# Kernel optimization log

Hardware: AMD Instinct MI355X
Metric: run time of the kernel (lower is better)

The kernel has to match this reference:

```python
import jax, jax.numpy as jnp
import numpy as np

DIM = 2048; H = 16; QLR = 512; KVLR = 512
NOPE = 128; ROPE = 64; VHD = 128
QKHD = NOPE + ROPE
SCALE = QKHD ** -0.5
EPS = 1.1920929e-07  # torch RMSNorm default eps = finfo(float32).eps
B = 1; S = 2048

def _rmsnorm(x, w):
    return x * jax.lax.rsqrt(jnp.mean(x * x, axis=-1, keepdims=True) + EPS) * w

def _rope(x, cos, sin):
    # x: [b, s, h, d]; cos/sin: [s, d//2] (consecutive-pair complex rotation)
    b, s, h, d = x.shape
    x2 = x.reshape(b, s, h, d // 2, 2)
    x0, x1 = x2[..., 0], x2[..., 1]
    c = cos[None, :, None, :]; sn = sin[None, :, None, :]
    y = jnp.stack([x0 * c - x1 * sn, x0 * sn + x1 * c], axis=-1)
    return y.reshape(b, s, h, d)

def setup_inputs() -> dict:
    key = jax.random.key(0)
    ks = jax.random.split(key, 12)
    def lin(k, fan_in, fan_out):
        bound = 1.0 / np.sqrt(fan_in)
        kw, kb = jax.random.split(k)
        w = jax.random.uniform(kw, (fan_out, fan_in), jnp.float32, -bound, bound)
        b = jax.random.uniform(kb, (fan_out,), jnp.float32, -bound, bound)
        return w, b
    x = jax.random.normal(ks[0], (B, S, DIM), jnp.float32)
    theta = jax.random.uniform(ks[1], (S, ROPE // 2), jnp.float32, 0.0, 2 * np.pi)
    freqs_cos = jnp.cos(theta); freqs_sin = jnp.sin(theta)
    mask = jnp.where(jnp.triu(jnp.ones((S, S), bool), k=1), jnp.float32(-1e9), jnp.float32(0.0))
    wq_a_w, wq_a_b = lin(ks[2], DIM, QLR)
    q_norm_w = jnp.ones((QLR,), jnp.float32)
    wq_b_w, wq_b_b = lin(ks[3], QLR, H * QKHD)
    wkv_a_w, wkv_a_b = lin(ks[4], DIM, KVLR + ROPE)
    kv_norm_w = jnp.ones((KVLR,), jnp.float32)
    wkv_b_w, wkv_b_b = lin(ks[5], KVLR, H * (NOPE + VHD))
    wo_w, wo_b = lin(ks[6], H * VHD, DIM)
    return {"x": x, "start_pos": 0, "freqs_cos": freqs_cos, "freqs_sin": freqs_sin,
            "mask": mask, "wq_a_w": wq_a_w, "wq_a_b": wq_a_b, "q_norm_w": q_norm_w,
            "wq_b_w": wq_b_w, "wq_b_b": wq_b_b, "wkv_a_w": wkv_a_w, "wkv_a_b": wkv_a_b,
            "kv_norm_w": kv_norm_w, "wkv_b_w": wkv_b_w, "wkv_b_b": wkv_b_b,
            "wo_w": wo_w, "wo_b": wo_b}

def reference(x, start_pos, freqs_cos, freqs_sin, mask,
              wq_a_w, wq_a_b, q_norm_w, wq_b_w, wq_b_b,
              wkv_a_w, wkv_a_b, kv_norm_w, wkv_b_w, wkv_b_b, wo_w, wo_b):
    bsz, seqlen, _ = x.shape
    # low-rank query: wq_b(q_norm(wq_a(x)))
    q = _rmsnorm(x @ wq_a_w.T + wq_a_b, q_norm_w) @ wq_b_w.T + wq_b_b
    q = q.reshape(bsz, seqlen, H, QKHD)
    q_nope, q_pe = q[..., :NOPE], q[..., NOPE:]
    q_pe = _rope(q_pe, freqs_cos, freqs_sin)
    kv = x @ wkv_a_w.T + wkv_a_b
    kv_lat, k_pe = kv[..., :KVLR], kv[..., KVLR:]
    k_pe = _rope(k_pe[:, :, None, :], freqs_cos, freqs_sin)  # [b,s,1,ROPE]
    q = jnp.concatenate([q_nope, q_pe], axis=-1)
    kvb = (_rmsnorm(kv_lat, kv_norm_w) @ wkv_b_w.T + wkv_b_b).reshape(bsz, seqlen, H, NOPE + VHD)
    k_nope, v = kvb[..., :NOPE], kvb[..., NOPE:]
    k = jnp.concatenate([k_nope, jnp.broadcast_to(k_pe, (bsz, seqlen, H, ROPE))], axis=-1)
    # prefill (start_pos=0): cache[:end_pos] == freshly written k/v
    scores = jnp.einsum('bshd,bthd->bsht', q, k) * SCALE
    scores = scores + mask[None, :, None, :]
    probs = jax.nn.softmax(scores.astype(jnp.float32), axis=-1).astype(x.dtype)
    out = jnp.einsum('bsht,bthd->bshd', probs, v).reshape(bsz, seqlen, H * VHD)
    return out @ wo_w.T + wo_b
```

## Files before the change

### kernel.cpp

```cpp
#include <hip/hip_runtime.h>
#include <hip/hip_bf16.h>

typedef __attribute__((ext_vector_type(8))) short short8x;
typedef __attribute__((ext_vector_type(4))) short short4x;
typedef __attribute__((ext_vector_type(4))) float float4x;
typedef __hip_bfloat16 bf16;

#define EPS_F 1.1920929e-07f
#define SCALE_F 0.07216878364870323f

__device__ inline float rdv(const void* p, size_t i, int f32) {
  return f32 ? ((const float*)p)[i] : __bfloat162float(((const bf16*)p)[i]);
}

__device__ inline int4 pack8(const float* s) {
  unsigned short h[8];
#pragma unroll
  for (int t = 0; t < 8; t++) {
    bf16 b = __float2bfloat16(s[t]);
    __builtin_memcpy(&h[t], &b, 2);
  }
  int4 r;
  r.x = (int)((unsigned)h[0] | ((unsigned)h[1] << 16));
  r.y = (int)((unsigned)h[2] | ((unsigned)h[3] << 16));
  r.z = (int)((unsigned)h[4] | ((unsigned)h[5] << 16));
  r.w = (int)((unsigned)h[6] | ((unsigned)h[7] << 16));
  return r;
}

typedef __attribute__((address_space(1))) const unsigned int gu32;
typedef __attribute__((address_space(3))) unsigned int lu32;
__device__ __forceinline__ void gload16(const void* g, void* l) {
  __builtin_amdgcn_global_load_lds((gu32*)g, (lu32*)l, 16, 0, 0);
}

__global__ __launch_bounds__(256) void detect_dtype(const unsigned short* __restrict__ x,
                                                    int* __restrict__ flag) {
  int tid = threadIdx.x;
  int cnt = 0;
#pragma unroll
  for (int i = 0; i < 4; i++) {
    unsigned short u = x[tid * 4 + i];
    int e = (u >> 7) & 0xFF;
    cnt += (e >= 118 && e <= 130) ? 1 : 0;
  }
#pragma unroll
  for (int off = 1; off < 64; off <<= 1) cnt += __shfl_xor(cnt, off);
  __shared__ int red[4];
  if ((tid & 63) == 0) red[tid >> 6] = cnt;
  __syncthreads();
  if (tid == 0) flag[0] = ((red[0] + red[1] + red[2] + red[3]) > 768) ? 0 : 1;
}

__global__ __launch_bounds__(256) void sentinel_kernel(bf16* out, int n) {
  int i = blockIdx.x * 256 + threadIdx.x;
  if (i < n) out[i] = __float2bfloat16(1000.0f);
}

template<int OMODE, bool A_DYN>
__device__ __forceinline__ void gemm128_body(
    const void* __restrict__ A, const void* __restrict__ W,
    const void* __restrict__ bias, void* __restrict__ Cout,
    int M, int N, int K, int f32in, int bx, int by,
    int kbeg, int kend, int addbias)
{
  __shared__ int4 As4[128 * 4];
  __shared__ int4 Bs4[128 * 4];
  const int tid = threadIdx.x, lane = tid & 63, wave = tid >> 6;
  const int grp = lane >> 4, l16 = lane & 15;
  const int m0 = bx * 128, n0 = by * 128;
  const int wm = (wave & 1) * 64, wn = (wave >> 1) * 64;
  float4x acc[4][4] = {};
  for (int k0 = kbeg; k0 < kend; k0 += 32) {
    if (!f32in) {
#pragma unroll
      for (int j = 0; j < 2; j++) {
        int row = wave * 32 + j * 16 + (lane >> 2);
        int cs = (lane & 3) ^ ((row >> 1) & 3);
        gload16((const bf16*)A + (size_t)(m0 + row) * K + k0 + cs * 8,
                &As4[(wave * 32 + j * 16) * 4]);
        gload16((const bf16*)W + (size_t)(n0 + row) * K + k0 + cs * 8,
                &Bs4[(wave * 32 + j * 16) * 4]);
      }
    } else {
#pragma unroll
      for (int i = 0; i < 2; i++) {
        int ch = tid + i * 256;
        int row = ch >> 2, c = ch & 3;
        int cs = c ^ ((row >> 1) & 3);
        size_t aoff = (size_t)(m0 + row) * K + k0 + cs * 8;
        size_t boff = (size_t)(n0 + row) * K + k0 + cs * 8;
        As4[row * 4 + c] = A_DYN ? pack8((const float*)A + aoff)
                                 : *(const int4*)((const bf16*)A + aoff);
        Bs4[row * 4 + c] = pack8((const float*)W + boff);
      }
    }
    __syncthreads();
    short8x af[4], bfr[4];
#pragma unroll
    for (int i = 0; i < 4; i++) {
      int ra = wm + i * 16 + l16;
      int rb = wn + i * 16 + l16;
      af[i]  = *(const short8x*)&As4[ra * 4 + (grp ^ ((ra >> 1) & 3))];
      bfr[i] = *(const short8x*)&Bs4[rb * 4 + (grp ^ ((rb >> 1) & 3))];
    }
#pragma unroll
    for (int i = 0; i < 4; i++)
#pragma unroll
      for (int j = 0; j < 4; j++)
        acc[i][j] = __builtin_amdgcn_mfma_f32_16x16x32_bf16(af[i], bfr[j], acc[i][j], 0, 0, 0);
    __syncthreads();
  }
#pragma unroll
  for (int j = 0; j < 4; j++) {
    int gn = n0 + wn + j * 16 + l16;
    float bv = addbias ? rdv(bias, gn, f32in) : 0.0f;
#pragma unroll
    for (int i = 0; i < 4; i++) {
      int gm0 = m0 + wm + i * 16 + grp * 4;
#pragma unroll
      for (int r = 0; r < 4; r++) {
        float v = acc[i][j][r] + bv;
        size_t idx = (size_t)(gm0 + r) * N + gn;
        if (OMODE == 0)      ((float*)Cout)[idx] = v;
        else if (OMODE == 1) ((bf16*)Cout)[idx] = __float2bfloat16(v);
        else {
          if (f32in) ((float*)Cout)[idx] = v;
          else       ((bf16*)Cout)[idx] = __float2bfloat16(v);
        }
      }
    }
  }
}

__global__ __launch_bounds__(256) void gemmB_dual(
    const void* __restrict__ A0, const void* __restrict__ A1,
    const void* __restrict__ W0, const void* __restrict__ W1,
    const void* __restrict__ b0, const void* __restrict__ b1,
    void* __restrict__ C0, void* __restrict__ C1,
    const int* __restrict__ flagp)
{
  const int z = blockIdx.z;
  if (z == 0 && blockIdx.y >= 24) return;
  const void* A = z ? A1 : A0;
  const void* W = z ? W1 : W0;
  const void* bias = z ? b1 : b0;
  void* C = z ? C1 : C0;
  const int N = z ? 4096 : 3072;
  gemm128_body<1, false>(A, W, bias, C, 2048, N, 512, flagp[0],
                         blockIdx.x, blockIdx.y, 0, 512, 1);
}

__global__ __launch_bounds__(256) void gemmWo_sk(
    const void* __restrict__ A, const void* __restrict__ W,
    const void* __restrict__ bias, float* __restrict__ part,
    const int* __restrict__ flagp)
{
  const int z = blockIdx.z;
  gemm128_body<0, false>(A, W, bias, part + (size_t)z * 2048 * 2048,
                         2048, 2048, 2048, flagp[0],
                         blockIdx.x, blockIdx.y, z * 1024, z * 1024 + 1024, z == 0);
}

__global__ __launch_bounds__(256) void reduce_out(
    const float* __restrict__ p0, const float* __restrict__ p1,
    void* __restrict__ out, const int* __restrict__ flagp)
{
  const int f32in = flagp[0];
  size_t i = ((size_t)blockIdx.x * 256 + threadIdx.x) * 4;
  float4 a = *(const float4*)(p0 + i);
  float4 b = *(const float4*)(p1 + i);
  a.x += b.x; a.y += b.y; a.z += b.z; a.w += b.w;
  if (f32in) {
    *(float4*)((float*)out + i) = a;
  } else {
    unsigned short h[4];
    bf16 t0 = __float2bfloat16(a.x); __builtin_memcpy(&h[0], &t0, 2);
    bf16 t1 = __float2bfloat16(a.y); __builtin_memcpy(&h[1], &t1, 2);
    bf16 t2 = __float2bfloat16(a.z); __builtin_memcpy(&h[2], &t2, 2);
    bf16 t3 = __float2bfloat16(a.w); __builtin_memcpy(&h[3], &t3, 2);
    int2 v;
    v.x = (int)((unsigned)h[0] | ((unsigned)h[1] << 16));
    v.y = (int)((unsigned)h[2] | ((unsigned)h[3] << 16));
    *(int2*)((bf16*)out + i) = v;
  }
}

template<int OMODE, bool A_DYN>
__device__ __forceinline__ void gemm64_body(
    const void* __restrict__ A, const void* __restrict__ W,
    const void* __restrict__ bias, void* __restrict__ Cout,
    int M, int N, int K, int f32in, int bx, int by,
    int kbeg, int kend, int addbias)
{
  __shared__ int4 As4[64 * 4];
  __shared__ int4 Bs4[64 * 4];
  const int tid = threadIdx.x, lane = tid & 63, wave = tid >> 6;
  const int grp = lane >> 4, l16 = lane & 15;
  const int m0 = bx * 64, n0 = by * 64;
  const int wm = (wave & 1) * 32, wn = (wave >> 1) * 32;
  float4x acc[2][2] = {};
  for (int k0 = kbeg; k0 < kend; k0 += 32) {
    if (!f32in) {
      int row = wave * 16 + (lane >> 2);
      int cs = (lane & 3) ^ ((row >> 1) & 3);
      gload16((const bf16*)A + (size_t)(m0 + row) * K + k0 + cs * 8,
              &As4[wave * 16 * 4]);
      gload16((const bf16*)W + (size_t)(n0 + row) * K + k0 + cs * 8,
              &Bs4[wave * 16 * 4]);
    } else {
      int row = tid >> 2, c = tid & 3;
      int cs = c ^ ((row >> 1) & 3);
      size_t aoff = (size_t)(m0 + row) * K + k0 + cs * 8;
      size_t boff = (size_t)(n0 + row) * K + k0 + cs * 8;
      As4[row * 4 + c] = A_DYN ? pack8((const float*)A + aoff)
                               : *(const int4*)((const bf16*)A + aoff);
      Bs4[row * 4 + c] = pack8((const float*)W + boff);
    }
    __syncthreads();
    short8x af[2], bfr[2];
#pragma unroll
    for (int i = 0; i < 2; i++) {
      int ra = wm + i * 16 + l16;
      int rb = wn + i * 16 + l16;
      af[i]  = *(const short8x*)&As4[ra * 4 + (grp ^ ((ra >> 1) & 3))];
      bfr[i] = *(const short8x*)&Bs4[rb * 4 + (grp ^ ((rb >> 1) & 3))];
    }
#pragma unroll
    for (int i = 0; i < 2; i++)
#pragma unroll
      for (int j = 0; j < 2; j++)
        acc[i][j] = __builtin_amdgcn_mfma_f32_16x16x32_bf16(af[i], bfr[j], acc[i][j], 0, 0, 0);
    __syncthreads();
  }
#pragma unroll
  for (int j = 0; j < 2; j++) {
    int gn = n0 + wn + j * 16 + l16;
    float bv = addbias ? rdv(bias, gn, f32in) : 0.0f;
#pragma unroll
    for (int i = 0; i < 2; i++) {
      int gm0 = m0 + wm + i * 16 + grp * 4;
#pragma unroll
      for (int r = 0; r < 4; r++) {
        float v = acc[i][j][r] + bv;
        size_t idx = (size_t)(gm0 + r) * N + gn;
        if (OMODE == 0)      ((float*)Cout)[idx] = v;
        else if (OMODE == 1) ((bf16*)Cout)[idx] = __float2bfloat16(v);
        else {
          if (f32in) ((float*)Cout)[idx] = v;
          else       ((bf16*)Cout)[idx] = __float2bfloat16(v);
        }
      }
    }
  }
}

__global__ __launch_bounds__(256) void gemmA_sk(
    const void* __restrict__ A,
    const void* __restrict__ W0, const void* __restrict__ W1,
    const void* __restrict__ b0, const void* __restrict__ b1,
    float* __restrict__ C0, float* __restrict__ C1,
    const int* __restrict__ flagp)
{
  const int z = blockIdx.z;
  const int mat = z >> 1, kh = z & 1;
  const int N = mat ? 576 : 512;
  if (blockIdx.y * 64 >= N) return;
  const void* W = mat ? W1 : W0;
  const void* bias = mat ? b1 : b0;
  float* C = (mat ? C1 : C0) + (size_t)kh * 2048 * N;
  gemm64_body<0, true>(A, W, bias, C, 2048, N, 2048, flagp[0],
                       blockIdx.x, blockIdx.y,
                       kh * 1024, kh * 1024 + 1024, kh == 0);
}

__global__ __launch_bounds__(256) void norms_merged(
    const float* __restrict__ q_a0, const float* __restrict__ q_a1,
    const float* __restrict__ kv_a0, const float* __restrict__ kv_a1,
    const void* __restrict__ qw, const void* __restrict__ kvw,
    const void* __restrict__ cosb, const void* __restrict__ sinb,
    bf16* __restrict__ qn, bf16* __restrict__ kvn, bf16* __restrict__ kpe,
    const int* __restrict__ flagp)
{
  const int f32in = flagp[0];
  const int b = blockIdx.x, tid = threadIdx.x;
  __shared__ float red[4];
  if (b < 2048) {
    const int s = b;
    size_t base = (size_t)s * 512;
    float v0 = q_a0[base + tid] + q_a1[base + tid];
    float v1 = q_a0[base + tid + 256] + q_a1[base + tid + 256];
    float ss = v0 * v0 + v1 * v1;
#pragma unroll
    for (int off = 1; off < 64; off <<= 1) ss += __shfl_xor(ss, off);
    if ((tid & 63) == 0) red[tid >> 6] = ss;
    __syncthreads();
    float tot = red[0] + red[1] + red[2] + red[3];
    float scale = rsqrtf(tot * (1.0f / 512.0f) + EPS_F);
    qn[base + tid]       = __float2bfloat16(v0 * scale * rdv(qw, tid, f32in));
    qn[base + tid + 256] = __float2bfloat16(v1 * scale * rdv(qw, tid + 256, f32in));
  } else {
    const int s = b - 2048;
    size_t base = (size_t)s * 576;
    float v0 = kv_a0[base + tid] + kv_a1[base + tid];
    float v1 = kv_a0[base + tid + 256] + kv_a1[base + tid + 256];
    float ss = v0 * v0 + v1 * v1;
#pragma unroll
    for (int off = 1; off < 64; off <<= 1) ss += __shfl_xor(ss, off);
    if ((tid & 63) == 0) red[tid >> 6] = ss;
    __syncthreads();
    float tot = red[0] + red[1] + red[2] + red[3];
    float scale = rsqrtf(tot * (1.0f / 512.0f) + EPS_F);
    kvn[(size_t)s * 512 + tid]       = __float2bfloat16(v0 * scale * rdv(kvw, tid, f32in));
    kvn[(size_t)s * 512 + tid + 256] = __float2bfloat16(v1 * scale * rdv(kvw, tid + 256, f32in));
    if (tid < 32) {
      float x0 = kv_a0[base + 512 + 2 * tid] + kv_a1[base + 512 + 2 * tid];
      float x1 = kv_a0[base + 512 + 2 * tid + 1] + kv_a1[base + 512 + 2 * tid + 1];
      float c  = rdv(cosb, (size_t)s * 32 + tid, f32in);
      float sn = rdv(sinb, (size_t)s * 32 + tid, f32in);
      kpe[s * 64 + 2 * tid]     = __float2bfloat16(x0 * c - x1 * sn);
      kpe[s * 64 + 2 * tid + 1] = __float2bfloat16(x0 * sn + x1 * c);
    }
  }
}

__global__ __launch_bounds__(256) void rope_vt_merged(
    bf16* __restrict__ q, const void* __restrict__ cosb,
    const void* __restrict__ sinb, const bf16* __restrict__ kvb,
    bf16* __restrict__ Vt, const int* __restrict__ flagp)
{
  const int b = blockIdx.x, tid = threadIdx.x;
  __shared__ __align__(16) bf16 tile[64][136];
  if (b < 2048) {
    const int f32in = flagp[0];
    const int s = b;
#pragma unroll
    for (int it = 0; it < 2; it++) {
      int p = tid + it * 256;
      int hh = p >> 5, jj = p & 31;
      bf16* src = q + (size_t)s * 3072 + hh * 192 + 128 + 2 * jj;
      float x0 = __bfloat162float(src[0]);
      float x1 = __bfloat162float(src[1]);
      float c  = rdv(cosb, (size_t)s * 32 + jj, f32in);
      float sn = rdv(sinb, (size_t)s * 32 + jj, f32in);
      src[0] = __float2bfloat16(x0 * c - x1 * sn);
      src[1] = __float2bfloat16(x0 * sn + x1 * c);
    }
  } else {
    const int hb = b - 2048;
    const int h = hb & 15;
    const int t0 = (hb >> 4) * 64;
#pragma unroll
    for (int i = 0; i < 4; i++) {
      int chunk = tid + i * 256;
      int row = chunk >> 4;
      int c8 = (chunk & 15) * 8;
      *(int4*)&tile[row][c8] =
          *(const int4*)(kvb + (size_t)(t0 + row) * 4096 + h * 256 + 128 + c8);
    }
    __syncthreads();
#pragma unroll
    for (int i = 0; i < 32; i++) {
      int idx = tid + i * 256;
      int d = idx >> 6;
      int t = idx & 63;
      Vt[((size_t)h * 128 + d) * 2048 + t0 + t] = tile[t][d];
    }
  }
}

__global__ __launch_bounds__(256) void attn_kernel(
    const bf16* __restrict__ Q, const bf16* __restrict__ kvb,
    const bf16* __restrict__ kpe, const bf16* __restrict__ Vt,
    bf16* __restrict__ Out)
{
  __shared__ __align__(16) bf16 Ks[64 * 200];
  __shared__ __align__(16) bf16 Vs[128 * 72];
  __shared__ __align__(16) bf16 plds[4][16 * 68];
  const int b = blockIdx.x;
  const int h = b & 15;
  const int tt = (b >> 4) & 15;
  const int q0 = ((b >> 8) ? (31 - tt) : tt) * 64;
  const int tid = threadIdx.x;
  const int wave = tid >> 6;
  const int lane = tid & 63;
  const int grp = lane >> 4, l16 = lane & 15;
  const int qrt = q0 + wave * 16;
  const bf16* Qbase = Q + (size_t)(qrt + l16) * 3072 + h * 192;
  short8x qf[6];
#pragma unroll
  for (int c = 0; c < 6; c++)
    qf[c] = *(const short8x*)(Qbase + c * 32 + grp * 8);
  float m_run[4], l_run[4];
  float4x o_acc[8] = {};
#pragma unroll
  for (int r = 0; r < 4; r++) { m_run[r] = -__builtin_inff(); l_run[r] = 0.f; }
  bf16* pl = &plds[wave][0];
  for (int t0 = 0; t0 <= q0; t0 += 64) {
#pragma unroll
    for (int i = 0; i < 4; i++) {
      int ch = tid + i * 256;
      int row = ch >> 4, c = ch & 15;
      *(int4*)&Ks[row * 200 + c * 8] =
          *(const int4*)(kvb + (size_t)(t0 + row) * 4096 + h * 256 + c * 8);
    }
#pragma unroll
    for (int i = 0; i < 2; i++) {
      int ch = tid + i * 256;
      int row = ch >> 3, c = ch & 7;
      *(int4*)&Ks[row * 200 + 128 + c * 8] =
          *(const int4*)(kpe + (size_t)(t0 + row) * 64 + c * 8);
    }
#pragma unroll
    for (int i = 0; i < 4; i++) {
      int ch = tid + i * 256;
      int row = ch >> 3, c = ch & 7;
      *(int4*)&Vs[row * 72 + c * 8] =
          *(const int4*)(Vt + ((size_t)h * 128 + row) * 2048 + t0 + c * 8);
    }
    __syncthreads();
    float4x sacc[4] = {};
#pragma unroll
    for (int n = 0; n < 4; n++) {
      const bf16* Kb = &Ks[(n * 16 + l16) * 200 + grp * 8];
#pragma unroll
      for (int c = 0; c < 6; c++) {
        short8x kf = *(const short8x*)(Kb + c * 32);
        sacc[n] = __builtin_amdgcn_mfma_f32_16x16x32_bf16(qf[c], kf, sacc[n], 0, 0, 0);
      }
    }
    float pv[4][4], alpha[4];
#pragma unroll
    for (int r = 0; r < 4; r++) {
      const int s_row = qrt + grp * 4 + r;
      float p0[4];
      float mx = -__builtin_inff();
#pragma unroll
      for (int n = 0; n < 4; n++) {
        int t = t0 + n * 16 + l16;
        float v = sacc[n][r] * SCALE_F;
        v = (t > s_row) ? -1.0e9f : v;
        p0[n] = v;
        mx = fmaxf(mx, v);
      }
      mx = fmaxf(mx, __shfl_xor(mx, 1));
      mx = fmaxf(mx, __shfl_xor(mx, 2));
      mx = fmaxf(mx, __shfl_xor(mx, 4));
      mx = fmaxf(mx, __shfl_xor(mx, 8));
      float m_new = fmaxf(m_run[r], mx);
      float a = __expf(m_run[r] - m_new);
      m_run[r] = m_new;
      float sum = 0.f;
#pragma unroll
      for (int n = 0; n < 4; n++) {
        float e = __expf(p0[n] - m_new);
        pv[n][r] = e;
        sum += e;
      }
      sum += __shfl_xor(sum, 1);
      sum += __shfl_xor(sum, 2);
      sum += __shfl_xor(sum, 4);
      sum += __shfl_xor(sum, 8);
      l_run[r] = l_run[r] * a + sum;
      alpha[r] = a;
    }
#pragma unroll
    for (int n = 0; n < 8; n++)
#pragma unroll
      for (int r = 0; r < 4; r++)
        o_acc[n][r] *= alpha[r];
#pragma unroll
    for (int n = 0; n < 4; n++)
#pragma unroll
      for (int r = 0; r < 4; r++)
        pl[(grp * 4 + r) * 68 + n * 16 + l16] = __float2bfloat16(pv[n][r]);
#pragma unroll
    for (int c = 0; c < 2; c++) {
      union { short4x h4[2]; short8x v8; } pk;
      const bf16* pp = pl + l16 * 68 + c * 32 + grp * 8;
      pk.h4[0] = *(const short4x*)(pp);
      pk.h4[1] = *(const short4x*)(pp + 4);
#pragma unroll
      for (int n = 0; n < 8; n++) {
        short8x vf = *(const short8x*)&Vs[(size_t)(n * 16 + l16) * 72 + c * 32 + grp * 8];
        o_acc[n] = __builtin_amdgcn_mfma_f32_16x16x32_bf16(pk.v8, vf, o_acc[n], 0, 0, 0);
      }
    }
    __syncthreads();
  }
  float inv[4];
#pragma unroll
  for (int r = 0; r < 4; r++) inv[r] = 1.0f / l_run[r];
#pragma unroll
  for (int n = 0; n < 8; n++)
#pragma unroll
    for (int r = 0; r < 4; r++) {
      int s_row = qrt + grp * 4 + r;
      Out[(size_t)s_row * 2048 + h * 128 + n * 16 + l16] =
          __float2bfloat16(o_acc[n][r] * inv[r]);
    }
}

extern "C" void kernel_launch(void* const* d_in, const int* in_sizes, int n_in,
                              void* d_out, int out_size, void* d_ws, size_t ws_size,
                              hipStream_t stream) {
  const void* x        = d_in[0];
  const void* fcos     = d_in[2];
  const void* fsin     = d_in[3];
  const void* wq_a_w   = d_in[5];
  const void* wq_a_b   = d_in[6];
  const void* q_norm_w = d_in[7];
  const void* wq_b_w   = d_in[8];
  const void* wq_b_b   = d_in[9];
  const void* wkv_a_w  = d_in[10];
  const void* wkv_a_b  = d_in[11];
  const void* kv_norm_w= d_in[12];
  const void* wkv_b_w  = d_in[13];
  const void* wkv_b_b  = d_in[14];
  const void* wo_w     = d_in[15];
  const void* wo_b     = d_in[16];

  const size_t KB = 1024, MB = 1024 * 1024;
  if (ws_size < 46 * MB) {
    sentinel_kernel<<<(out_size + 255) / 256, 256, 0, stream>>>((bf16*)d_out, out_size);
    return;
  }
  char* ws = (char*)d_ws;
  bf16*  kpe    = (bf16*)(ws);
  int*   flag   = (int*)(ws + 256 * KB);
  bf16*  qbuf   = (bf16*)(ws + 512 * KB);
  bf16*  kvb    = (bf16*)(ws + 12 * MB + 512 * KB);
  bf16*  Vt     = (bf16*)(ws + 28 * MB + 512 * KB);
  bf16*  attnout= (bf16*)(ws + 36 * MB + 512 * KB);
  float* kv_a0  = (float*)(ws + 512 * KB);
  float* kv_a1  = (float*)(ws + 5 * MB);
  float* q_a0   = (float*)(ws + 36 * MB + 512 * KB);
  float* q_a1   = (float*)(ws + 40 * MB + 512 * KB);
  bf16*  qn     = (bf16*)(ws + 28 * MB + 512 * KB);
  bf16*  kvn    = (bf16*)(ws + 30 * MB + 512 * KB);
  float* wpart  = (float*)(ws + 512 * KB);

  dim3 blk(256);
  detect_dtype<<<1, blk, 0, stream>>>((const unsigned short*)x, flag);
  gemmA_sk<<<dim3(32, 9, 4), blk, 0, stream>>>(
      x, wq_a_w, wkv_a_w, wq_a_b, wkv_a_b, q_a0, kv_a0, flag);
  norms_merged<<<4096, blk, 0, stream>>>(
      q_a0, q_a1, kv_a0, kv_a1, q_norm_w, kv_norm_w, fcos, fsin,
      qn, kvn, kpe, flag);
  gemmB_dual<<<dim3(16, 32, 2), blk, 0, stream>>>(
      qn, kvn, wq_b_w, wkv_b_w, wq_b_b, wkv_b_b, qbuf, kvb, flag);
  rope_vt_merged<<<2560, blk, 0, stream>>>(qbuf, fcos, fsin, kvb, Vt, flag);
  attn_kernel<<<dim3(512), blk, 0, stream>>>(qbuf, kvb, kpe, Vt, attnout);
  gemmWo_sk<<<dim3(16, 16, 2), blk, 0, stream>>>(attnout, wo_w, wo_b, wpart, flag);
  reduce_out<<<4096, blk, 0, stream>>>(wpart, wpart + (size_t)2048 * 2048, d_out, flag);
}
```

Measured before the change: 349.2 us.

## Prefetch next K/V tile into registers and use lazy softmax rescaling in attention

The attention loop now issues global loads for the next K, k_pe and V tile into registers before computing on the current tile, then writes them to shared memory after the PV MFMAs. This hides global load latency behind compute. The online softmax rescales the output accumulator only when some row max grows by more than 8, which skips most alpha multiplies at the cost of bounded fp32 growth. The change also adds s_setprio around the MFMA sections and launch_bounds(256,2), which raise register pressure and add an extra barrier per iteration.

```diff
diff --git a/kernel.cpp b/kernel.cpp
--- a/kernel.cpp
+++ b/kernel.cpp
@@ -369,7 +369,7 @@
   }
 }
 
-__global__ __launch_bounds__(256) void attn_kernel(
+__global__ __launch_bounds__(256, 2) void attn_kernel(
     const bf16* __restrict__ Q, const bf16* __restrict__ kvb,
     const bf16* __restrict__ kpe, const bf16* __restrict__ Vt,
     bf16* __restrict__ Out)
@@ -386,40 +386,56 @@
   const int lane = tid & 63;
   const int grp = lane >> 4, l16 = lane & 15;
   const int qrt = q0 + wave * 16;
+  const int krow = tid >> 4, kcol8 = (tid & 15) * 8;
+  const int prow = tid >> 3, pcol8 = (tid & 7) * 8;
+
   const bf16* Qbase = Q + (size_t)(qrt + l16) * 3072 + h * 192;
   short8x qf[6];
 #pragma unroll
   for (int c = 0; c < 6; c++)
     qf[c] = *(const short8x*)(Qbase + c * 32 + grp * 8);
+
+  int4 kReg[4], peReg[2], vReg[4];
+
+  auto attn_issue = [&](int T0) {
+#pragma unroll
+    for (int i = 0; i < 4; i++)
+      kReg[i] = *(const int4*)(kvb + (size_t)(T0 + krow + i * 16) * 4096 + h * 256 + kcol8);
+#pragma unroll
+    for (int i = 0; i < 2; i++)
+      peReg[i] = *(const int4*)(kpe + (size_t)(T0 + prow + i * 32) * 64 + pcol8);
+#pragma unroll
+    for (int i = 0; i < 4; i++)
+      vReg[i] = *(const int4*)(Vt + ((size_t)h * 128 + prow + i * 32) * 2048 + T0 + pcol8);
+  };
+  auto attn_write = [&]() {
+#pragma unroll
+    for (int i = 0; i < 4; i++)
+      *(int4*)&Ks[(krow + i * 16) * 200 + kcol8] = kReg[i];
+#pragma unroll
+    for (int i = 0; i < 2; i++)
+      *(int4*)&Ks[(prow + i * 32) * 200 + 128 + pcol8] = peReg[i];
+#pragma unroll
+    for (int i = 0; i < 4; i++)
+      *(int4*)&Vs[(prow + i * 32) * 72 + pcol8] = vReg[i];
+  };
+
   float m_run[4], l_run[4];
   float4x o_acc[8] = {};
 #pragma unroll
   for (int r = 0; r < 4; r++) { m_run[r] = -__builtin_inff(); l_run[r] = 0.f; }
   bf16* pl = &plds[wave][0];
+
+  attn_issue(0);
+  attn_write();
+  __syncthreads();
+
   for (int t0 = 0; t0 <= q0; t0 += 64) {
-#pragma unroll
-    for (int i = 0; i < 4; i++) {
-      int ch = tid + i * 256;
-      int row = ch >> 4, c = ch & 15;
-      *(int4*)&Ks[row * 200 + c * 8] =
-          *(const int4*)(kvb + (size_t)(t0 + row) * 4096 + h * 256 + c * 8);
-    }
-#pragma unroll
-    for (int i = 0; i < 2; i++) {
-      int ch = tid + i * 256;
-      int row = ch >> 3, c = ch & 7;
-      *(int4*)&Ks[row * 200 + 128 + c * 8] =
-          *(const int4*)(kpe + (size_t)(t0 + row) * 64 + c * 8);
-    }
-#pragma unroll
-    for (int i = 0; i < 4; i++) {
-      int ch = tid + i * 256;
-      int row = ch >> 3, c = ch & 7;
-      *(int4*)&Vs[row * 72 + c * 8] =
-          *(const int4*)(Vt + ((size_t)h * 128 + row) * 2048 + t0 + c * 8);
-    }
-    __syncthreads();
+    const bool more = (t0 + 64 <= q0);
+    if (more) attn_issue(t0 + 64);
+
     float4x sacc[4] = {};
+    __builtin_amdgcn_s_setprio(1);
 #pragma unroll
     for (int n = 0; n < 4; n++) {
       const bf16* Kb = &Ks[(n * 16 + l16) * 200 + grp * 8];
@@ -429,31 +445,51 @@
         sacc[n] = __builtin_amdgcn_mfma_f32_16x16x32_bf16(qf[c], kf, sacc[n], 0, 0, 0);
       }
     }
-    float pv[4][4], alpha[4];
+    __builtin_amdgcn_s_setprio(0);
+
+    float p0[4][4], mxv[4];
+    int grow = 0;
 #pragma unroll
     for (int r = 0; r < 4; r++) {
       const int s_row = qrt + grp * 4 + r;
-      float p0[4];
       float mx = -__builtin_inff();
 #pragma unroll
       for (int n = 0; n < 4; n++) {
         int t = t0 + n * 16 + l16;
         float v = sacc[n][r] * SCALE_F;
         v = (t > s_row) ? -1.0e9f : v;
-        p0[n] = v;
+        p0[r][n] = v;
         mx = fmaxf(mx, v);
       }
       mx = fmaxf(mx, __shfl_xor(mx, 1));
       mx = fmaxf(mx, __shfl_xor(mx, 2));
       mx = fmaxf(mx, __shfl_xor(mx, 4));
       mx = fmaxf(mx, __shfl_xor(mx, 8));
-      float m_new = fmaxf(m_run[r], mx);
-      float a = __expf(m_run[r] - m_new);
-      m_run[r] = m_new;
+      mxv[r] = mx;
+      grow |= (mx > m_run[r] + 8.0f) ? 1 : 0;
+    }
+    if (__any(grow)) {
+      float alpha[4];
+#pragma unroll
+      for (int r = 0; r < 4; r++) {
+        float mn = fmaxf(m_run[r], mxv[r]);
+        alpha[r] = __expf(m_run[r] - mn);
+        m_run[r] = mn;
+        l_run[r] *= alpha[r];
+      }
+#pragma unroll
+      for (int n = 0; n < 8; n++)
+#pragma unroll
+        for (int r = 0; r < 4; r++)
+          o_acc[n][r] *= alpha[r];
+    }
+    float pv[4][4];
+#pragma unroll
+    for (int r = 0; r < 4; r++) {
       float sum = 0.f;
 #pragma unroll
       for (int n = 0; n < 4; n++) {
-        float e = __expf(p0[n] - m_new);
+        float e = __expf(p0[r][n] - m_run[r]);
         pv[n][r] = e;
         sum += e;
       }
@@ -461,19 +497,15 @@
       sum += __shfl_xor(sum, 2);
       sum += __shfl_xor(sum, 4);
       sum += __shfl_xor(sum, 8);
-      l_run[r] = l_run[r] * a + sum;
-      alpha[r] = a;
-    }
-#pragma unroll
-    for (int n = 0; n < 8; n++)
-#pragma unroll
-      for (int r = 0; r < 4; r++)
-        o_acc[n][r] *= alpha[r];
+      l_run[r] += sum;
+    }
 #pragma unroll
     for (int n = 0; n < 4; n++)
 #pragma unroll
       for (int r = 0; r < 4; r++)
         pl[(grp * 4 + r) * 68 + n * 16 + l16] = __float2bfloat16(pv[n][r]);
+
+    __builtin_amdgcn_s_setprio(1);
 #pragma unroll
     for (int c = 0; c < 2; c++) {
       union { short4x h4[2]; short8x v8; } pk;
@@ -486,7 +518,13 @@
         o_acc[n] = __builtin_amdgcn_mfma_f32_16x16x32_bf16(pk.v8, vf, o_acc[n], 0, 0, 0);
       }
     }
-    __syncthreads();
+    __builtin_amdgcn_s_setprio(0);
+
+    if (more) {
+      __syncthreads();
+      attn_write();
+      __syncthreads();
+    }
   }
   float inv[4];
 #pragma unroll
```

New measurement: 429.3 us. 1.23x slower.
